# Performance work log

Measured on AMD Instinct MI355X. Metric: run time of the kernel, lower is better.

The kernel has to match this reference:

```python
import jax, jax.numpy as jnp
import numpy as np

B = 65536      # graphs per batch
NPG = 8        # nodes per graph (row_cluster has 8 entries)
N = B * NPG    # total nodes
P = 3 * B      # pooled nodes (3 row-clusters per graph)


def setup_inputs() -> dict:
    key = jax.random.key(0)
    ks = jax.random.split(key, 10)
    # per-graph edge template (undirected -> both directions); rows: {0,1,2},{3,4,5},{6,7}
    pairs = np.array([(0, 1), (1, 2), (0, 3), (3, 4), (4, 5), (3, 6), (6, 7), (2, 5), (5, 7), (1, 7)], dtype=np.int64)
    und = np.concatenate([pairs, pairs[:, ::-1]], axis=0)              # [20,2]
    off = (np.arange(B, dtype=np.int64) * NPG)[:, None, None]
    ei = (und[None] + off).reshape(-1, 2).T                            # [2, 20B]
    # pooled edges = avg_pool's coalesced cluster graph: triangle on 3 clusters per graph
    ppairs = np.array([(0, 1), (1, 2), (0, 2)], dtype=np.int64)
    pund = np.concatenate([ppairs, ppairs[:, ::-1]], axis=0)           # [6,2]
    poff = (np.arange(B, dtype=np.int64) * 3)[:, None, None]
    ei2 = (pund[None] + poff).reshape(-1, 2).T                         # [2, 6B]
    # consecutive-relabelled cluster assignment (PyG: 3*batch + [1,1,1,2,2,2,3,3] -> 0..3B-1)
    cluster = np.tile(np.array([0, 0, 0, 1, 1, 1, 2, 2], dtype=np.int64), B) + np.repeat(np.arange(B, dtype=np.int64) * 3, NPG)
    batch2 = np.arange(P, dtype=np.int64) // 3

    def lin(k, fan_in, fan_out):
        kw, kb = jax.random.split(k)
        s = 1.0 / np.sqrt(fan_in)
        W = jax.random.uniform(kw, (fan_in, fan_out), minval=-s, maxval=s, dtype=jnp.float32)
        b = jax.random.uniform(kb, (fan_out,), minval=-s, maxval=s, dtype=jnp.float32)
        return W, b

    W1, b1 = lin(ks[0], 336, 100)
    W2, b2 = lin(ks[1], 100, 100)
    W3, b3 = lin(ks[2], 100, 100)
    W4, b4 = lin(ks[3], 100, 100)
    W5, b5 = lin(ks[4], 100, 100)
    L1w, L1b = lin(ks[5], 100, 100)
    L2w, L2b = lin(ks[6], 100, 100)
    L3w, L3b = lin(ks[7], 100, 29)
    x = jax.random.normal(ks[8], (N, 336), dtype=jnp.float32)
    return dict(x=x, edge_index=jnp.asarray(ei), edge_index2=jnp.asarray(ei2),
                cluster=jnp.asarray(cluster), batch2=jnp.asarray(batch2),
                W1=W1, b1=b1, W2=W2, b2=b2, W3=W3, b3=b3, W4=W4, b4=b4, W5=W5, b5=b5,
                L1w=L1w, L1b=L1b, L2w=L2w, L2b=L2b, L3w=L3w, L3b=L3b)


def gcn(x, ei, W, b, n):
    # PyG GCNConv: x' = D^{-1/2}(A+I)D^{-1/2} (x W) + b
    h = x @ W
    loop = jnp.arange(n)
    s = jnp.concatenate([ei[0], loop])
    d = jnp.concatenate([ei[1], loop])
    deg = jax.ops.segment_sum(jnp.ones(s.shape[0], h.dtype), d, num_segments=n)
    dinv = jax.lax.rsqrt(deg)  # deg >= 1 because of self-loops
    norm = dinv[s] * dinv[d]
    return jax.ops.segment_sum(h[s] * norm[:, None], d, num_segments=n) + b


def reference(x, edge_index, edge_index2, cluster, batch2,
              W1, b1, W2, b2, W3, b3, W4, b4, W5, b5,
              L1w, L1b, L2w, L2b, L3w, L3b):
    h = jax.nn.relu(gcn(x, edge_index, W1, b1, N))
    h = jax.nn.relu(gcn(h, edge_index, W2, b2, N))
    h = jax.nn.relu(gcn(h, edge_index, W3, b3, N))
    # avg_pool: mean node features per cluster -> [P, 100]
    cnt = jax.ops.segment_sum(jnp.ones(N, h.dtype), cluster, num_segments=P)
    hp = jax.ops.segment_sum(h, cluster, num_segments=P) / cnt[:, None]
    hp = jax.nn.relu(gcn(hp, edge_index2, W4, b4, P))
    hp = jax.nn.relu(gcn(hp, edge_index2, W5, b5, P))
    # global_mean_pool over pooled-graph batch -> [B, 100]
    cnt2 = jax.ops.segment_sum(jnp.ones(P, hp.dtype), batch2, num_segments=B)
    g = jax.ops.segment_sum(hp, batch2, num_segments=B) / cnt2[:, None]
    g = jax.nn.relu(g @ L1w + L1b)
    g = jax.nn.relu(g @ L2w + L2b)
    return g @ L3w + L3b
```

## Files before the change

kernel.cpp:

```cpp
#include <hip/hip_runtime.h>


typedef __bf16 bf16_t;
typedef bf16_t bf16x8 __attribute__((ext_vector_type(8)));
typedef unsigned short u16x8 __attribute__((ext_vector_type(8)));
typedef float f32x4 __attribute__((ext_vector_type(4)));

#define C_ 0.28867513459481287f
#define T_ (1.0f/3.0f)
#define Q_ 0.25f

#define OFF_W1  0
#define OFF_W2  39424
#define OFF_W3  53760
#define OFF_W4  68096
#define OFF_W5  82432
#define OFF_L1W 96768
#define OFF_L2W 111104
#define OFF_L3W 125440
#define WS_ELEMS 129536

__device__ __forceinline__ unsigned short f2bf(float f) {
  return __builtin_bit_cast(unsigned short, (__bf16)f);
}
__device__ __forceinline__ float bf2f(unsigned short h) {
  unsigned u = ((unsigned)h) << 16;
  return __builtin_bit_cast(float, u);
}

__global__ __launch_bounds__(256) void prep_w(
    const float* __restrict__ W1, const float* __restrict__ W2,
    const float* __restrict__ W3, const float* __restrict__ W4,
    const float* __restrict__ W5, const float* __restrict__ L1w,
    const float* __restrict__ L2w, const float* __restrict__ L3w,
    unsigned short* __restrict__ ws)
{
  const int bid = blockIdx.x;
  int m, ct;
  if (bid < 7)       { m = 0; ct = bid; }
  else if (bid < 49) { m = 1 + (bid - 7) / 7; ct = (bid - 7) % 7; }
  else               { m = 7; ct = bid - 49; }
  const float* W; int K, NC, KSF; int off;
  switch (m) {
    case 0:  W = W1;  K = 336; NC = 100; KSF = 11; off = OFF_W1;  break;
    case 1:  W = W2;  K = 100; NC = 100; KSF = 4;  off = OFF_W2;  break;
    case 2:  W = W3;  K = 100; NC = 100; KSF = 4;  off = OFF_W3;  break;
    case 3:  W = W4;  K = 100; NC = 100; KSF = 4;  off = OFF_W4;  break;
    case 4:  W = W5;  K = 100; NC = 100; KSF = 4;  off = OFF_W5;  break;
    case 5:  W = L1w; K = 100; NC = 100; KSF = 4;  off = OFF_L1W; break;
    case 6:  W = L2w; K = 100; NC = 100; KSF = 4;  off = OFF_L2W; break;
    default: W = L3w; K = 100; NC = 29;  KSF = 4;  off = OFF_L3W; break;
  }
  for (int task = threadIdx.x; task < KSF * 64; task += 256) {
    const int ks = task >> 6, lane = task & 63;
    const int col = ct * 16 + (lane & 15);
    u16x8 o;
#pragma unroll
    for (int j = 0; j < 8; ++j) {
      const int k = ks * 32 + (lane >> 4) * 8 + j;
      const float v = (k < K && col < NC) ? W[(size_t)k * NC + col] : 0.f;
      o[j] = f2bf(v);
    }
    *(u16x8*)(ws + off + (size_t)(ct * KSF + ks) * 512 + (size_t)lane * 8) = o;
  }
}

#define MFMA1(ACC, AH, BH)                                                     \
  ACC = __builtin_amdgcn_mfma_f32_16x16x32_bf16(                               \
      __builtin_bit_cast(bf16x8, AH), __builtin_bit_cast(bf16x8, BH), ACC,     \
      0, 0, 0)

#define MFMA2S(ACC, AH, AL, BH)                                                \
  do {                                                                         \
    MFMA1(ACC, AH, BH);                                                        \
    MFMA1(ACC, AL, BH);                                                        \
  } while (0)

#define LOADB(MOFF, KSF_, CT, KS, BH)                                          \
  BH = *(const u16x8*)(ws + (MOFF) +                                           \
                       (size_t)((CT) * (KSF_) + (KS)) * 512 + lane8)

#define STORE_H(R, Cc, V)                                                      \
  do {                                                                         \
    const unsigned short hb_ = f2bf(V);                                        \
    const int pb_ = (R) * 256 + ((((Cc) * 2)) ^ (((R) & 7) << 4));             \
    *(unsigned short*)(Ahi + pb_) = hb_;                                       \
  } while (0)

#define DENSE_KLOOP(MOFF)                                                      \
  do {                                                                         \
    _Pragma("unroll")                                                          \
    for (int rt = 0; rt < 2; ++rt)                                             \
      _Pragma("unroll")                                                        \
      for (int ct = 0; ct < 7; ++ct) acc[rt][ct] = (f32x4){0.f, 0.f, 0.f, 0.f};\
    _Pragma("unroll 1")                                                        \
    for (int ks = 0; ks < 4; ++ks) {                                           \
      u16x8 ah[2];                                                             \
      _Pragma("unroll")                                                        \
      for (int rt = 0; rt < 2; ++rt) {                                         \
        const int row = w32 + rt * 16 + l15;                                   \
        const int pb = row * 256 + ((ks * 64 + q16) ^ ((row & 7) << 4));       \
        ah[rt] = *(const u16x8*)(Ahi + pb);                                    \
      }                                                                        \
      _Pragma("unroll")                                                        \
      for (int ct = 0; ct < 7; ++ct) {                                         \
        u16x8 bh;                                                              \
        LOADB(MOFF, 4, ct, ks, bh);                                            \
        MFMA1(acc[0][ct], ah[0], bh);                                          \
        MFMA1(acc[1][ct], ah[1], bh);                                          \
      }                                                                        \
    }                                                                          \
  } while (0)

#define EPI_MIX(BOFF, DOPOOL)                                                  \
  do {                                                                         \
    __syncthreads();                                                           \
    _Pragma("unroll")                                                          \
    for (int rt = 0; rt < 2; ++rt) {                                           \
      _Pragma("unroll")                                                        \
      for (int ct = 0; ct < 7; ++ct) {                                         \
        const float v0 = acc[rt][ct][0], v1 = acc[rt][ct][1];                  \
        const float v2 = acc[rt][ct][2], v3 = acc[rt][ct][3];                  \
        const float u0 = __shfl_xor(v0, 16), u1 = __shfl_xor(v1, 16);          \
        const float u2 = __shfl_xor(v2, 16), u3 = __shfl_xor(v3, 16);          \
        float o0, o1, o2, o3;                                                  \
        if (!p1) {       \
          o0 = T_ * v0 + C_ * (v1 + v3);                                       \
          o1 = C_ * (v0 + v2) + Q_ * (v1 + u3);                                \
          o2 = T_ * v2 + C_ * (v1 + u1);                                       \
          o3 = Q_ * v3 + C_ * (v0 + u0 + u2);                                  \
        } else {         \
          o0 = T_ * v0 + C_ * (u3 + v1);                                       \
          o1 = Q_ * (v1 + v3) + C_ * (v0 + u2);                                \
          o2 = T_ * v2 + C_ * (u3 + v3);                                       \
          o3 = Q_ * (v3 + v1 + u1) + C_ * v2;                                  \
        }                                                                      \
        const int col = ct * 16 + l15;                                         \
        const float bv = bs[(BOFF) + col];                                     \
        float h0 = fmaxf(o0 + bv, 0.f), h1 = fmaxf(o1 + bv, 0.f);              \
        float h2 = fmaxf(o2 + bv, 0.f), h3 = fmaxf(o3 + bv, 0.f);              \
        if (col >= 100) { h0 = h1 = h2 = h3 = 0.f; }                           \
        if (DOPOOL) {                                                          \
          float pp = p1 ? ((h0 + h1) * (1.f/9.f) + (h2 + h3) * (1.f/6.f))      \
                        : ((h0 + h1 + h2 + h3) * (1.f/9.f));                   \
          pp += __shfl_xor(pp, 16);                                            \
          if (!p1) {                                                           \
            const int g = 4 * w + 2 * rt + (q >> 1);                           \
            STORE_H(g, col, pp);                                               \
          }                                                                    \
        } else {                                                               \
          const int rb = w32 + rt * 16 + 4 * q;                                \
          STORE_H(rb + 0, col, h0); STORE_H(rb + 1, col, h1);                  \
          STORE_H(rb + 2, col, h2); STORE_H(rb + 3, col, h3);                  \
        }                                                                      \
      }                                                                        \
    }                                                                          \
    __syncthreads();                                                           \
  } while (0)

#define CHAIN_LAYER(MOFF, BOFF)                                                \
  do {                                                                         \
    f32x4 c0 = {0.f, 0.f, 0.f, 0.f}, c1 = {0.f, 0.f, 0.f, 0.f};                \
    const int ct0 = w, ct1 = w + 4;                                            \
    _Pragma("unroll")                                                          \
    for (int ks = 0; ks < 4; ++ks) {                                           \
      const int row = l15;                                                     \
      const int pb = row * 256 + ((ks * 64 + q16) ^ ((row & 7) << 4));         \
      const u16x8 ah = *(const u16x8*)(Ahi + pb);                              \
      u16x8 bh;                                                                \
      LOADB(MOFF, 4, ct0, ks, bh);  MFMA1(c0, ah, bh);                         \
      if (w < 3) { LOADB(MOFF, 4, ct1, ks, bh); MFMA1(c1, ah, bh); }           \
    }                                                                          \
    __syncthreads();                                                           \
    _Pragma("unroll")                                                          \
    for (int i = 0; i < 4; ++i) {                                              \
      const int row = 4 * q + i;                                               \
      {                                                                        \
        const int col = ct0 * 16 + l15;                                        \
        float hv = fmaxf(c0[i] + bs[(BOFF) + col], 0.f);                       \
        if (col >= 100) hv = 0.f;                                              \
        STORE_H(row, col, hv);                                                 \
      }                                                                        \
      if (w < 3) {                                                             \
        const int col = ct1 * 16 + l15;                                        \
        float hv = fmaxf(c1[i] + bs[(BOFF) + col], 0.f);                       \
        if (col >= 100) hv = 0.f;                                              \
        STORE_H(row, col, hv);                                                 \
      }                                                                        \
    }                                                                          \
    __syncthreads();                                                           \
  } while (0)

__global__ __launch_bounds__(256, 3)
void rownet_mfma(const float* __restrict__ x,
                 const unsigned short* __restrict__ ws,
                 const float* __restrict__ b1, const float* __restrict__ b2,
                 const float* __restrict__ b3, const float* __restrict__ b4,
                 const float* __restrict__ b5, const float* __restrict__ L1b,
                 const float* __restrict__ L2b, const float* __restrict__ L3b,
                 float* __restrict__ out)
{
  __shared__ __align__(16) unsigned char smem[35712];
  unsigned char* const Ahi = smem;
  float* const bs = (float*)(smem + 32768);

  const int tid  = threadIdx.x;
  const int w    = tid >> 6;
  const int lane = tid & 63;
  const int l15  = lane & 15;
  const int q    = lane >> 4;
  const int q16  = q * 16;
  const int p1   = q & 1;
  const int lane8 = lane * 8;
  const int w32  = w * 32;
  const int g0   = blockIdx.x * 16;
  const int n0   = blockIdx.x * 128;

  if (tid < 100) {
    bs[      tid] = b1[tid];  bs[100 + tid] = b2[tid];
    bs[200 + tid] = b3[tid];  bs[300 + tid] = b4[tid];
    bs[400 + tid] = b5[tid];  bs[500 + tid] = L1b[tid];
    bs[600 + tid] = L2b[tid];
  }
  if (tid < 29) bs[700 + tid] = L3b[tid];

  f32x4 acc[2][7];

  {
    const float* const xb =
        x + (size_t)(n0 + w32 + l15) * 336 + q * 8;
    const bool qlow = (q < 2);
#pragma unroll
    for (int rt = 0; rt < 2; ++rt)
#pragma unroll
      for (int ct = 0; ct < 7; ++ct) acc[rt][ct] = (f32x4){0.f, 0.f, 0.f, 0.f};

#pragma unroll 1
    for (int ks = 0; ks < 11; ++ks) {
      u16x8 ah[2], al[2];
#pragma unroll
      for (int rt = 0; rt < 2; ++rt) {
        float4 p0, p1v;
        if (ks < 10 || qlow) {
          const float* xr = xb + (size_t)rt * (16 * 336) + ks * 32;
          p0  = *(const float4*)xr;
          p1v = *(const float4*)(xr + 4);
        } else {
          p0 = make_float4(0.f, 0.f, 0.f, 0.f);
          p1v = p0;
        }
        const float v[8] = {p0.x, p0.y, p0.z, p0.w, p1v.x, p1v.y, p1v.z, p1v.w};
#pragma unroll
        for (int j = 0; j < 8; ++j) {
          const unsigned short hb = f2bf(v[j]);
          ah[rt][j] = hb;
          al[rt][j] = f2bf(v[j] - bf2f(hb));
        }
      }
#pragma unroll
      for (int ct = 0; ct < 7; ++ct) {
        u16x8 bh;
        LOADB(OFF_W1, 11, ct, ks, bh);
#pragma unroll
        for (int rt = 0; rt < 2; ++rt)
          MFMA2S(acc[rt][ct], ah[rt], al[rt], bh);
      }
    }
  }
  {
    const int row = tid & 127;
    const int half = tid >> 7;
    const int pb = row * 256 + ((224 + 16 * half) ^ ((row & 7) << 4));
    *(u16x8*)(Ahi + pb) = (u16x8){0, 0, 0, 0, 0, 0, 0, 0};
  }

  EPI_MIX(0, false);

  DENSE_KLOOP(OFF_W2);  EPI_MIX(100, false);
  DENSE_KLOOP(OFF_W3);  EPI_MIX(200, true);

  CHAIN_LAYER(OFF_W4, 300);
  CHAIN_LAYER(OFF_W5, 400);
  CHAIN_LAYER(OFF_L1W, 500);
  CHAIN_LAYER(OFF_L2W, 600);

  if (w < 2) {
    f32x4 c0 = {0.f, 0.f, 0.f, 0.f};
#pragma unroll
    for (int ks = 0; ks < 4; ++ks) {
      const int row = l15;
      const int pb = row * 256 + ((ks * 64 + q16) ^ ((row & 7) << 4));
      const u16x8 ah = *(const u16x8*)(Ahi + pb);
      u16x8 bh0;
      LOADB(OFF_L3W, 4, w, ks, bh0);
      MFMA1(c0, ah, bh0);
    }
    const int col = w * 16 + l15;
#pragma unroll
    for (int i = 0; i < 4; ++i) {
      if (col < 29)
        out[(size_t)(g0 + 4 * q + i) * 29 + col] = c0[i] + bs[700 + col];
    }
  }
}

extern "C" void kernel_launch(void* const* d_in, const int* in_sizes, int n_in,
                              void* d_out, int out_size, void* d_ws, size_t ws_size,
                              hipStream_t stream) {
  (void)in_sizes; (void)n_in; (void)out_size; (void)ws_size;
  const float* x   = (const float*)d_in[0];
  const float* W1  = (const float*)d_in[5];
  const float* b1  = (const float*)d_in[6];
  const float* W2  = (const float*)d_in[7];
  const float* b2  = (const float*)d_in[8];
  const float* W3  = (const float*)d_in[9];
  const float* b3  = (const float*)d_in[10];
  const float* W4  = (const float*)d_in[11];
  const float* b4  = (const float*)d_in[12];
  const float* W5  = (const float*)d_in[13];
  const float* b5  = (const float*)d_in[14];
  const float* L1w = (const float*)d_in[15];
  const float* L1b = (const float*)d_in[16];
  const float* L2w = (const float*)d_in[17];
  const float* L2b = (const float*)d_in[18];
  const float* L3w = (const float*)d_in[19];
  const float* L3b = (const float*)d_in[20];
  unsigned short* ws = (unsigned short*)d_ws;

  prep_w<<<51, 256, 0, stream>>>(W1, W2, W3, W4, W5, L1w, L2w, L3w, ws);
  rownet_mfma<<<4096, 256, 0, stream>>>(x, ws, b1, b2, b3, b4, b5,
                                        L1b, L2b, L3b, (float*)d_out);
}
```

Baseline: 321.8 us.

## Split per-graph tail MLP into separate kernel with full 128-row MFMA tiles

After: 304.5 us. -5.4%, faster.

```diff
diff --git a/kernel.cpp b/kernel.cpp
--- a/kernel.cpp
+++ b/kernel.cpp
@@ -18,7 +18,7 @@
 #define OFF_L1W 96768
 #define OFF_L2W 111104
 #define OFF_L3W 125440
-#define WS_ELEMS 129536
+#define M_OFF_BYTES 262144
 
 __device__ __forceinline__ unsigned short f2bf(float f) {
   return __builtin_bit_cast(unsigned short, (__bf16)f);
@@ -112,7 +112,7 @@
     }                                                                          \
   } while (0)
 
-#define EPI_MIX(BOFF, DOPOOL)                                                  \
+#define EPI_MIX(BOFF)                                                          \
   do {                                                                         \
     __syncthreads();                                                           \
     _Pragma("unroll")                                                          \
@@ -124,12 +124,12 @@
         const float u0 = __shfl_xor(v0, 16), u1 = __shfl_xor(v1, 16);          \
         const float u2 = __shfl_xor(v2, 16), u3 = __shfl_xor(v3, 16);          \
         float o0, o1, o2, o3;                                                  \
-        if (!p1) {       \
+        if (!p1) {            \
           o0 = T_ * v0 + C_ * (v1 + v3);                                       \
           o1 = C_ * (v0 + v2) + Q_ * (v1 + u3);                                \
           o2 = T_ * v2 + C_ * (v1 + u1);                                       \
           o3 = Q_ * v3 + C_ * (v0 + u0 + u2);                                  \
-        } else {         \
+        } else {              \
           o0 = T_ * v0 + C_ * (u3 + v1);                                       \
           o1 = Q_ * (v1 + v3) + C_ * (v0 + u2);                                \
           o2 = T_ * v2 + C_ * (u3 + v3);                                       \
@@ -140,67 +140,22 @@
         float h0 = fmaxf(o0 + bv, 0.f), h1 = fmaxf(o1 + bv, 0.f);              \
         float h2 = fmaxf(o2 + bv, 0.f), h3 = fmaxf(o3 + bv, 0.f);              \
         if (col >= 100) { h0 = h1 = h2 = h3 = 0.f; }                           \
-        if (DOPOOL) {                                                          \
-          float pp = p1 ? ((h0 + h1) * (1.f/9.f) + (h2 + h3) * (1.f/6.f))      \
-                        : ((h0 + h1 + h2 + h3) * (1.f/9.f));                   \
-          pp += __shfl_xor(pp, 16);                                            \
-          if (!p1) {                                                           \
-            const int g = 4 * w + 2 * rt + (q >> 1);                           \
-            STORE_H(g, col, pp);                                               \
-          }                                                                    \
-        } else {                                                               \
-          const int rb = w32 + rt * 16 + 4 * q;                                \
-          STORE_H(rb + 0, col, h0); STORE_H(rb + 1, col, h1);                  \
-          STORE_H(rb + 2, col, h2); STORE_H(rb + 3, col, h3);                  \
-        }                                                                      \
+        const int rb = w32 + rt * 16 + 4 * q;                                  \
+        STORE_H(rb + 0, col, h0); STORE_H(rb + 1, col, h1);                    \
+        STORE_H(rb + 2, col, h2); STORE_H(rb + 3, col, h3);                    \
       }                                                                        \
     }                                                                          \
     __syncthreads();                                                           \
   } while (0)
 
-#define CHAIN_LAYER(MOFF, BOFF)                                                \
-  do {                                                                         \
-    f32x4 c0 = {0.f, 0.f, 0.f, 0.f}, c1 = {0.f, 0.f, 0.f, 0.f};                \
-    const int ct0 = w, ct1 = w + 4;                                            \
-    _Pragma("unroll")                                                          \
-    for (int ks = 0; ks < 4; ++ks) {                                           \
-      const int row = l15;                                                     \
-      const int pb = row * 256 + ((ks * 64 + q16) ^ ((row & 7) << 4));         \
-      const u16x8 ah = *(const u16x8*)(Ahi + pb);                              \
-      u16x8 bh;                                                                \
-      LOADB(MOFF, 4, ct0, ks, bh);  MFMA1(c0, ah, bh);                         \
-      if (w < 3) { LOADB(MOFF, 4, ct1, ks, bh); MFMA1(c1, ah, bh); }           \
-    }                                                                          \
-    __syncthreads();                                                           \
-    _Pragma("unroll")                                                          \
-    for (int i = 0; i < 4; ++i) {                                              \
-      const int row = 4 * q + i;                                               \
-      {                                                                        \
-        const int col = ct0 * 16 + l15;                                        \
-        float hv = fmaxf(c0[i] + bs[(BOFF) + col], 0.f);                       \
-        if (col >= 100) hv = 0.f;                                              \
-        STORE_H(row, col, hv);                                                 \
-      }                                                                        \
-      if (w < 3) {                                                             \
-        const int col = ct1 * 16 + l15;                                        \
-        float hv = fmaxf(c1[i] + bs[(BOFF) + col], 0.f);                       \
-        if (col >= 100) hv = 0.f;                                              \
-        STORE_H(row, col, hv);                                                 \
-      }                                                                        \
-    }                                                                          \
-    __syncthreads();                                                           \
-  } while (0)
-
 __global__ __launch_bounds__(256, 3)
-void rownet_mfma(const float* __restrict__ x,
+void rownet_node(const float* __restrict__ x,
                  const unsigned short* __restrict__ ws,
+                 unsigned char* __restrict__ mws,
                  const float* __restrict__ b1, const float* __restrict__ b2,
-                 const float* __restrict__ b3, const float* __restrict__ b4,
-                 const float* __restrict__ b5, const float* __restrict__ L1b,
-                 const float* __restrict__ L2b, const float* __restrict__ L3b,
-                 float* __restrict__ out)
+                 const float* __restrict__ b3)
 {
-  __shared__ __align__(16) unsigned char smem[35712];
+  __shared__ __align__(16) unsigned char smem[33984];
   unsigned char* const Ahi = smem;
   float* const bs = (float*)(smem + 32768);
 
@@ -217,12 +172,10 @@
   const int n0   = blockIdx.x * 128;
 
   if (tid < 100) {
-    bs[      tid] = b1[tid];  bs[100 + tid] = b2[tid];
-    bs[200 + tid] = b3[tid];  bs[300 + tid] = b4[tid];
-    bs[400 + tid] = b5[tid];  bs[500 + tid] = L1b[tid];
-    bs[600 + tid] = L2b[tid];
-  }
-  if (tid < 29) bs[700 + tid] = L3b[tid];
+    bs[      tid] = b1[tid];
+    bs[100 + tid] = b2[tid];
+    bs[200 + tid] = b3[tid];
+  }
 
   f32x4 acc[2][7];
 
@@ -274,33 +227,149 @@
     *(u16x8*)(Ahi + pb) = (u16x8){0, 0, 0, 0, 0, 0, 0, 0};
   }
 
-  EPI_MIX(0, false);
-
-  DENSE_KLOOP(OFF_W2);  EPI_MIX(100, false);
-  DENSE_KLOOP(OFF_W3);  EPI_MIX(200, true);
-
-  CHAIN_LAYER(OFF_W4, 300);
-  CHAIN_LAYER(OFF_W5, 400);
-  CHAIN_LAYER(OFF_L1W, 500);
-  CHAIN_LAYER(OFF_L2W, 600);
-
-  if (w < 2) {
-    f32x4 c0 = {0.f, 0.f, 0.f, 0.f};
+  EPI_MIX(0);
+
+  DENSE_KLOOP(OFF_W2);  EPI_MIX(100);
+  DENSE_KLOOP(OFF_W3);
+
+#pragma unroll
+  for (int rt = 0; rt < 2; ++rt) {
+#pragma unroll
+    for (int ct = 0; ct < 7; ++ct) {
+      const float v0 = acc[rt][ct][0], v1 = acc[rt][ct][1];
+      const float v2 = acc[rt][ct][2], v3 = acc[rt][ct][3];
+      const float u0 = __shfl_xor(v0, 16), u1 = __shfl_xor(v1, 16);
+      const float u2 = __shfl_xor(v2, 16), u3 = __shfl_xor(v3, 16);
+      float o0, o1, o2, o3;
+      if (!p1) {
+        o0 = T_ * v0 + C_ * (v1 + v3);
+        o1 = C_ * (v0 + v2) + Q_ * (v1 + u3);
+        o2 = T_ * v2 + C_ * (v1 + u1);
+        o3 = Q_ * v3 + C_ * (v0 + u0 + u2);
+      } else {
+        o0 = T_ * v0 + C_ * (u3 + v1);
+        o1 = Q_ * (v1 + v3) + C_ * (v0 + u2);
+        o2 = T_ * v2 + C_ * (u3 + v3);
+        o3 = Q_ * (v3 + v1 + u1) + C_ * v2;
+      }
+      const int col = ct * 16 + l15;
+      const float bv = bs[200 + col];
+      float h0 = fmaxf(o0 + bv, 0.f), h1 = fmaxf(o1 + bv, 0.f);
+      float h2 = fmaxf(o2 + bv, 0.f), h3 = fmaxf(o3 + bv, 0.f);
+      if (col >= 100) { h0 = h1 = h2 = h3 = 0.f; }
+      float pp = p1 ? ((h0 + h1) * (1.f/9.f) + (h2 + h3) * (1.f/6.f))
+                    : ((h0 + h1 + h2 + h3) * (1.f/9.f));
+      pp += __shfl_xor(pp, 16);
+      if (!p1 && col < 100) {
+        const int g_abs = g0 + 4 * w + 2 * rt + (q >> 1);
+        const int blk2 = g_abs >> 7, r2 = g_abs & 127;
+        const size_t byte = (size_t)blk2 * 32768 + r2 * 256
+                          + ((col * 2) ^ ((r2 & 7) << 4));
+        *(unsigned short*)(mws + byte) = f2bf(pp);
+      }
+    }
+  }
+}
+
+#define EPI_PLAIN(BOFF)                                                        \
+  do {                                                                         \
+    _Pragma("unroll")                                                          \
+    for (int rt = 0; rt < 2; ++rt) {                                           \
+      _Pragma("unroll")                                                        \
+      for (int ct = 0; ct < 7; ++ct) {                                         \
+        const int col = ct * 16 + l15;                                         \
+        const float bv = bs[(BOFF) + col];                                     \
+        _Pragma("unroll")                                                      \
+        for (int i = 0; i < 4; ++i) {                                          \
+          float hv = fmaxf(acc[rt][ct][i] + bv, 0.f);                          \
+          if (col >= 100) hv = 0.f;                                            \
+          STORE_H(w32 + rt * 16 + 4 * q + i, col, hv);                         \
+        }                                                                      \
+      }                                                                        \
+    }                                                                          \
+  } while (0)
+
+__global__ __launch_bounds__(256, 3)
+void rownet_tail(const unsigned short* __restrict__ ws,
+                 const unsigned char* __restrict__ mws,
+                 const float* __restrict__ b4, const float* __restrict__ b5,
+                 const float* __restrict__ L1b, const float* __restrict__ L2b,
+                 const float* __restrict__ L3b,
+                 float* __restrict__ out)
+{
+  __shared__ __align__(16) unsigned char smem[34496];
+  unsigned char* const Ahi = smem;
+  float* const bs = (float*)(smem + 32768);
+
+  const int tid  = threadIdx.x;
+  const int w    = tid >> 6;
+  const int lane = tid & 63;
+  const int l15  = lane & 15;
+  const int q    = lane >> 4;
+  const int q16  = q * 16;
+  const int lane8 = lane * 8;
+  const int w32  = w * 32;
+
+  {
+    const unsigned char* src = mws + (size_t)blockIdx.x * 32768;
+#pragma unroll
+    for (int it = 0; it < 8; ++it) {
+      const int off = (it * 256 + tid) * 16;
+      *(u16x8*)(Ahi + off) = *(const u16x8*)(src + off);
+    }
+  }
+  if (tid < 100) {
+    bs[      tid] = b4[tid];
+    bs[100 + tid] = b5[tid];
+    bs[200 + tid] = L1b[tid];
+    bs[300 + tid] = L2b[tid];
+  }
+  if (tid < 29) bs[400 + tid] = L3b[tid];
+  __syncthreads();
+
+  f32x4 acc[2][7];
+  DENSE_KLOOP(OFF_W4);  EPI_PLAIN(0);
+  DENSE_KLOOP(OFF_W5);  EPI_PLAIN(100);
+  DENSE_KLOOP(OFF_L1W); EPI_PLAIN(200);
+  DENSE_KLOOP(OFF_L2W); EPI_PLAIN(300);
+
+  {
+    f32x4 c[2][2];
+#pragma unroll
+    for (int rt = 0; rt < 2; ++rt)
+#pragma unroll
+      for (int ct = 0; ct < 2; ++ct) c[rt][ct] = (f32x4){0.f, 0.f, 0.f, 0.f};
 #pragma unroll
     for (int ks = 0; ks < 4; ++ks) {
-      const int row = l15;
-      const int pb = row * 256 + ((ks * 64 + q16) ^ ((row & 7) << 4));
-      const u16x8 ah = *(const u16x8*)(Ahi + pb);
-      u16x8 bh0;
-      LOADB(OFF_L3W, 4, w, ks, bh0);
-      MFMA1(c0, ah, bh0);
+      u16x8 ah[2];
+#pragma unroll
+      for (int rt = 0; rt < 2; ++rt) {
+        const int row = w32 + rt * 16 + l15;
+        const int pb = row * 256 + ((ks * 64 + q16) ^ ((row & 7) << 4));
+        ah[rt] = *(const u16x8*)(Ahi + pb);
+      }
+#pragma unroll
+      for (int ct = 0; ct < 2; ++ct) {
+        u16x8 bh;
+        LOADB(OFF_L3W, 4, ct, ks, bh);
+        MFMA1(c[0][ct], ah[0], bh);
+        MFMA1(c[1][ct], ah[1], bh);
+      }
     }
-    const int col = w * 16 + l15;
-#pragma unroll
-    for (int i = 0; i < 4; ++i) {
-      if (col < 29)
-        out[(size_t)(g0 + 4 * q + i) * 29 + col] = c0[i] + bs[700 + col];
-    }
+    const size_t gbase = (size_t)blockIdx.x * 128;
+#pragma unroll
+    for (int rt = 0; rt < 2; ++rt)
+#pragma unroll
+      for (int ct = 0; ct < 2; ++ct) {
+        const int col = ct * 16 + l15;
+        if (col < 29) {
+#pragma unroll
+          for (int i = 0; i < 4; ++i) {
+            const int row = w32 + rt * 16 + 4 * q + i;
+            out[(gbase + row) * 29 + col] = c[rt][ct][i] + bs[400 + col];
+          }
+        }
+      }
   }
 }
 
@@ -326,8 +395,10 @@
   const float* L3w = (const float*)d_in[19];
   const float* L3b = (const float*)d_in[20];
   unsigned short* ws = (unsigned short*)d_ws;
+  unsigned char* mws = (unsigned char*)d_ws + M_OFF_BYTES;
 
   prep_w<<<51, 256, 0, stream>>>(W1, W2, W3, W4, W5, L1w, L2w, L3w, ws);
-  rownet_mfma<<<4096, 256, 0, stream>>>(x, ws, b1, b2, b3, b4, b5,
-                                        L1b, L2b, L3b, (float*)d_out);
-}
+  rownet_node<<<4096, 256, 0, stream>>>(x, ws, mws, b1, b2, b3);
+  rownet_tail<<<512, 256, 0, stream>>>(ws, mws, b4, b5, L1b, L2b, L3b,
+                                       (float*)d_out);
+}
```
